# Kernel optimization log

Measured on AMD Instinct MI355X. Metric: run time of the kernel, lower is better.

Reference implementation:

```python
import jax, jax.numpy as jnp
import numpy as np
from jax import lax

RADIUS = 2

def make_kernels(radius):
    # Faithfully reproduces the torch __init__, INCLUDING the bug where
    # NE is computed from the already-normalized NW and SE from SW.
    r = radius
    k = 2 * r + 1
    w = np.ones((k, k), dtype=np.float32)
    L = w.copy(); L[:, r + 1:] = 0
    R = w.copy(); R[:, :r] = 0
    U = w.copy(); U[r + 1:, :] = 0
    D = w.copy(); D[:r, :] = 0
    NW, NE, SW, SE = U.copy(), U.copy(), D.copy(), D.copy()
    half = (r + 1) * k
    L = L / half; R = R / half; U = U / half; D = D / half
    NW[:, r + 1:] = 0
    NE[:, :r] = 0
    SW[:, r + 1:] = 0
    SE[:, :r] = 0
    NW = NW / (r + 1) ** 2
    NE = NW / (r + 1) ** 2  # bug in original: uses new NW
    SW = SW / (r + 1) ** 2
    SE = SW / (r + 1) ** 2  # bug in original: uses new SW
    # order matches d channels 0..7 in forward: L,R,U,D,NW,NE,SW,SE
    return jnp.asarray(np.stack([L, R, U, D, NW, NE, SW, SE])[:, None])  # [8,1,k,k]

def setup_inputs() -> dict:
    key = jax.random.key(0)
    x = jax.random.uniform(key, (8, 3, 768, 768), dtype=jnp.float32)
    return {"x": x, "kernels": make_kernels(RADIUS), "iteration": 3}

def reference(x, kernels, iteration):
    B, C, H, W = x.shape
    k = kernels.shape[-1]
    r = (k - 1) // 2
    # fuse the per-channel loop: treat each (image, channel) as its own sample
    xc = x.reshape(B * C, 1, H, W)

    def step(xc, _):
        # all 8 directional box filters in one conv: [BC,8,H,W]
        conv = lax.conv_general_dilated(
            xc, kernels, window_strides=(1, 1), padding=[(r, r), (r, r)],
            dimension_numbers=("NCHW", "OIHW", "NCHW"))
        d = conv - xc                                   # [BC,8,H,W]
        idx = jnp.argmin(jnp.abs(d), axis=1, keepdims=True)
        dm = jnp.take_along_axis(d, idx, axis=1)        # [BC,1,H,W]
        return xc + dm, None

    xc, _ = lax.scan(step, xc, None, length=iteration)
    return xc.reshape(B, C, H, W)
```

## Files before the change

kernel.cpp:

```cpp
#include <hip/hip_runtime.h>
#include <math.h>


typedef float f4 __attribute__((ext_vector_type(4)));

#define TW 64
#define TH 24

template<int H2, int W2, bool LAST>
__device__ __forceinline__ void step(const float* __restrict__ X,
                                     float* __restrict__ Y,
                                     float* __restrict__ outp,
                                     int gy0, int gx0, int tid) {
    constexpr int PW = W2 + 4;
    const float w15 = 1.0f / 15.0f;
    const float w9  = 1.0f / 9.0f;
    const float w81 = (1.0f / 9.0f) / 9.0f;

    constexpr int SC = W2 / 4;
    constexpr int NSEG = H2 * SC;
    for (int s = tid; s < NSEG; s += 256) {
        const int y  = s / SC;
        const int xs = (s - y * SC) * 4;
        float Wv[5][8];
        #pragma unroll
        for (int r = 0; r < 5; r++) {
            const float* p = X + (y + r) * PW + xs;
            *(f4*)&Wv[r][0] = *(const f4*)p;
            *(f4*)&Wv[r][4] = *(const f4*)(p + 4);
        }
        #pragma unroll
        for (int j = 0; j < 4; j++) {
            const float c = Wv[2][j + 2];
            float aL = 0.0f, aR = 0.0f, aU = 0.0f, aD = 0.0f;
            float aNW = 0.0f, aNE = 0.0f, aSW = 0.0f, aSE = 0.0f;
            #pragma unroll
            for (int r = 0; r < 5; r++)
                #pragma unroll
                for (int cc = 0; cc < 3; cc++)
                    aL = fmaf(w15, Wv[r][j + cc], aL);
            #pragma unroll
            for (int r = 0; r < 5; r++)
                #pragma unroll
                for (int cc = 2; cc < 5; cc++)
                    aR = fmaf(w15, Wv[r][j + cc], aR);
            #pragma unroll
            for (int r = 0; r < 3; r++)
                #pragma unroll
                for (int cc = 0; cc < 5; cc++)
                    aU = fmaf(w15, Wv[r][j + cc], aU);
            #pragma unroll
            for (int r = 2; r < 5; r++)
                #pragma unroll
                for (int cc = 0; cc < 5; cc++)
                    aD = fmaf(w15, Wv[r][j + cc], aD);
            #pragma unroll
            for (int r = 0; r < 3; r++)
                #pragma unroll
                for (int cc = 0; cc < 3; cc++) {
                    aNW = fmaf(w9,  Wv[r][j + cc], aNW);
                    aNE = fmaf(w81, Wv[r][j + cc], aNE);
                }
            #pragma unroll
            for (int r = 2; r < 5; r++)
                #pragma unroll
                for (int cc = 0; cc < 3; cc++) {
                    aSW = fmaf(w9,  Wv[r][j + cc], aSW);
                    aSE = fmaf(w81, Wv[r][j + cc], aSE);
                }

            const float d0 = aL - c, d1 = aR - c, d2 = aU - c, d3 = aD - c;
            const float d4 = aNW - c, d5 = aNE - c, d6 = aSW - c, d7 = aSE - c;

            float best = fabsf(d0), bd = d0, a;
            a = fabsf(d1); if (a < best) { best = a; bd = d1; }
            a = fabsf(d2); if (a < best) { best = a; bd = d2; }
            a = fabsf(d3); if (a < best) { best = a; bd = d3; }
            a = fabsf(d4); if (a < best) { best = a; bd = d4; }
            a = fabsf(d5); if (a < best) { best = a; bd = d5; }
            a = fabsf(d6); if (a < best) { best = a; bd = d6; }
            a = fabsf(d7); if (a < best) { best = a; bd = d7; }

            const float res = c + bd;
            if (LAST) {
                outp[y * 768 + xs + j] = res;
            } else {
                const bool inside = ((unsigned)(gy0 + y) < 768u) &&
                                    ((unsigned)(gx0 + xs + j) < 768u);
                Y[y * W2 + xs + j] = inside ? res : 0.0f;
            }
        }
    }
    __syncthreads();
}

__global__ __launch_bounds__(256) void swf_fused(const float* __restrict__ in,
                                                 float* __restrict__ out) {
    __shared__ __align__(16) float A[36 * 76];
    __shared__ __align__(16) float B[32 * 72];

    const int tid = threadIdx.x;
    const int tx0 = blockIdx.x * TW;
    const int ty0 = blockIdx.y * TH;
    const long long base = (long long)blockIdx.z * (768 * 768);
    const float* inp = in + base;

    for (int i = tid; i < 36 * 76; i += 256) {
        int ly = i / 76, lx = i - ly * 76;
        int gy = ty0 + ly - 6, gx = tx0 + lx - 6;
        float v = 0.0f;
        if ((unsigned)gy < 768u && (unsigned)gx < 768u)
            v = inp[gy * 768 + gx];
        A[i] = v;
    }
    __syncthreads();

    step<32, 72, false>(A, B, nullptr, ty0 - 4, tx0 - 4, tid);
    step<28, 68, false>(B, A, nullptr, ty0 - 2, tx0 - 2, tid);
    step<24, 64, true >(A, nullptr,
                        out + base + (long long)ty0 * 768 + tx0, ty0, tx0, tid);
}

extern "C" void kernel_launch(void* const* d_in, const int* in_sizes, int n_in,
                              void* d_out, int out_size, void* d_ws, size_t ws_size,
                              hipStream_t stream) {
    const float* x = (const float*)d_in[0];
    float* out = (float*)d_out;

    dim3 grid(768 / TW, 768 / TH, 24);
    dim3 block(256);
    swf_fused<<<grid, block, 0, stream>>>(x, out);
}
```

Baseline: 208.6 us.

## Enlarge fused tile to 64x64, vectorize loads/stores, restructure per-row accumulation

Raises tile height from 24 to 64 so the halo recomputation overhead of the three fused iterations shrinks, growing shared memory to 76x76 and 72x72 buffers. Loads the input tile with 2-wide vector reads, writes results as float4, and skips bounds masking for interior tiles. The filter sums are accumulated row by row into 8x4 accumulators and the argmin becomes a tree reduction. The larger shared footprint (about 43KB) and more registers per thread may reduce occupancy, and the grid has fewer blocks.

```diff
diff --git a/kernel.cpp b/kernel.cpp
--- a/kernel.cpp
+++ b/kernel.cpp
@@ -2,10 +2,11 @@
 #include <math.h>
 
 
-typedef float f4 __attribute__((ext_vector_type(4)));
+typedef float f4v __attribute__((ext_vector_type(4)));
+typedef float f2v __attribute__((ext_vector_type(2), aligned(8)));
 
 #define TW 64
-#define TH 24
+#define TH 64
 
 template<int H2, int W2, bool LAST>
 __device__ __forceinline__ void step(const float* __restrict__ X,
@@ -13,82 +14,103 @@
                                      float* __restrict__ outp,
                                      int gy0, int gx0, int tid) {
     constexpr int PW = W2 + 4;
+    constexpr int SC = W2 / 4;
+    constexpr int NSEG = H2 * SC;
     const float w15 = 1.0f / 15.0f;
     const float w9  = 1.0f / 9.0f;
     const float w81 = (1.0f / 9.0f) / 9.0f;
 
-    constexpr int SC = W2 / 4;
-    constexpr int NSEG = H2 * SC;
+    const bool interior = (gy0 >= 0) && (gx0 >= 0) &&
+                          (gy0 + H2 <= 768) && (gx0 + W2 <= 768);
+
     for (int s = tid; s < NSEG; s += 256) {
         const int y  = s / SC;
         const int xs = (s - y * SC) * 4;
-        float Wv[5][8];
+        const float* rp = X + y * PW + xs;
+
+        float acc[8][4];
+        #pragma unroll
+        for (int d = 0; d < 8; d++)
+            #pragma unroll
+            for (int j = 0; j < 4; j++) acc[d][j] = 0.0f;
+        float ctr[4];
+
         #pragma unroll
         for (int r = 0; r < 5; r++) {
-            const float* p = X + (y + r) * PW + xs;
-            *(f4*)&Wv[r][0] = *(const f4*)p;
-            *(f4*)&Wv[r][4] = *(const f4*)(p + 4);
+            const float* p = rp + r * PW;
+            f4v lo = *(const f4v*)p;
+            f4v hi = *(const f4v*)(p + 4);
+            float w[8] = {lo.x, lo.y, lo.z, lo.w, hi.x, hi.y, hi.z, hi.w};
+
+            #pragma unroll
+            for (int j = 0; j < 4; j++) {
+                acc[0][j] = fmaf(w15, w[j + 0], acc[0][j]);
+                acc[0][j] = fmaf(w15, w[j + 1], acc[0][j]);
+                acc[0][j] = fmaf(w15, w[j + 2], acc[0][j]);
+                acc[1][j] = fmaf(w15, w[j + 2], acc[1][j]);
+                acc[1][j] = fmaf(w15, w[j + 3], acc[1][j]);
+                acc[1][j] = fmaf(w15, w[j + 4], acc[1][j]);
+                if (r < 3) {
+                    acc[2][j] = fmaf(w15, w[j + 0], acc[2][j]);
+                    acc[2][j] = fmaf(w15, w[j + 1], acc[2][j]);
+                    acc[2][j] = fmaf(w15, w[j + 2], acc[2][j]);
+                    acc[2][j] = fmaf(w15, w[j + 3], acc[2][j]);
+                    acc[2][j] = fmaf(w15, w[j + 4], acc[2][j]);
+                    acc[4][j] = fmaf(w9,  w[j + 0], acc[4][j]);
+                    acc[4][j] = fmaf(w9,  w[j + 1], acc[4][j]);
+                    acc[4][j] = fmaf(w9,  w[j + 2], acc[4][j]);
+                    acc[5][j] = fmaf(w81, w[j + 0], acc[5][j]);
+                    acc[5][j] = fmaf(w81, w[j + 1], acc[5][j]);
+                    acc[5][j] = fmaf(w81, w[j + 2], acc[5][j]);
+                }
+                if (r >= 2) {
+                    acc[3][j] = fmaf(w15, w[j + 0], acc[3][j]);
+                    acc[3][j] = fmaf(w15, w[j + 1], acc[3][j]);
+                    acc[3][j] = fmaf(w15, w[j + 2], acc[3][j]);
+                    acc[3][j] = fmaf(w15, w[j + 3], acc[3][j]);
+                    acc[3][j] = fmaf(w15, w[j + 4], acc[3][j]);
+                    acc[6][j] = fmaf(w9,  w[j + 0], acc[6][j]);
+                    acc[6][j] = fmaf(w9,  w[j + 1], acc[6][j]);
+                    acc[6][j] = fmaf(w9,  w[j + 2], acc[6][j]);
+                    acc[7][j] = fmaf(w81, w[j + 0], acc[7][j]);
+                    acc[7][j] = fmaf(w81, w[j + 1], acc[7][j]);
+                    acc[7][j] = fmaf(w81, w[j + 2], acc[7][j]);
+                }
+                if (r == 2) ctr[j] = w[j + 2];
+            }
         }
+
+        f4v R;
         #pragma unroll
         for (int j = 0; j < 4; j++) {
-            const float c = Wv[2][j + 2];
-            float aL = 0.0f, aR = 0.0f, aU = 0.0f, aD = 0.0f;
-            float aNW = 0.0f, aNE = 0.0f, aSW = 0.0f, aSE = 0.0f;
-            #pragma unroll
-            for (int r = 0; r < 5; r++)
-                #pragma unroll
-                for (int cc = 0; cc < 3; cc++)
-                    aL = fmaf(w15, Wv[r][j + cc], aL);
-            #pragma unroll
-            for (int r = 0; r < 5; r++)
-                #pragma unroll
-                for (int cc = 2; cc < 5; cc++)
-                    aR = fmaf(w15, Wv[r][j + cc], aR);
-            #pragma unroll
-            for (int r = 0; r < 3; r++)
-                #pragma unroll
-                for (int cc = 0; cc < 5; cc++)
-                    aU = fmaf(w15, Wv[r][j + cc], aU);
-            #pragma unroll
-            for (int r = 2; r < 5; r++)
-                #pragma unroll
-                for (int cc = 0; cc < 5; cc++)
-                    aD = fmaf(w15, Wv[r][j + cc], aD);
-            #pragma unroll
-            for (int r = 0; r < 3; r++)
-                #pragma unroll
-                for (int cc = 0; cc < 3; cc++) {
-                    aNW = fmaf(w9,  Wv[r][j + cc], aNW);
-                    aNE = fmaf(w81, Wv[r][j + cc], aNE);
-                }
-            #pragma unroll
-            for (int r = 2; r < 5; r++)
-                #pragma unroll
-                for (int cc = 0; cc < 3; cc++) {
-                    aSW = fmaf(w9,  Wv[r][j + cc], aSW);
-                    aSE = fmaf(w81, Wv[r][j + cc], aSE);
-                }
+            const float c = ctr[j];
+            const float e0 = acc[0][j] - c, e1 = acc[1][j] - c;
+            const float e2 = acc[2][j] - c, e3 = acc[3][j] - c;
+            const float e4 = acc[4][j] - c, e5 = acc[5][j] - c;
+            const float e6 = acc[6][j] - c, e7 = acc[7][j] - c;
+            float m01 = (fabsf(e1) < fabsf(e0)) ? e1 : e0;
+            float m23 = (fabsf(e3) < fabsf(e2)) ? e3 : e2;
+            float m45 = (fabsf(e5) < fabsf(e4)) ? e5 : e4;
+            float m67 = (fabsf(e7) < fabsf(e6)) ? e7 : e6;
+            float mA  = (fabsf(m23) < fabsf(m01)) ? m23 : m01;
+            float mB  = (fabsf(m67) < fabsf(m45)) ? m67 : m45;
+            float bd  = (fabsf(mB)  < fabsf(mA))  ? mB  : mA;
+            const float res = c + bd;
+            if (j == 0) R.x = res; else if (j == 1) R.y = res;
+            else if (j == 2) R.z = res; else R.w = res;
+        }
 
-            const float d0 = aL - c, d1 = aR - c, d2 = aU - c, d3 = aD - c;
-            const float d4 = aNW - c, d5 = aNE - c, d6 = aSW - c, d7 = aSE - c;
-
-            float best = fabsf(d0), bd = d0, a;
-            a = fabsf(d1); if (a < best) { best = a; bd = d1; }
-            a = fabsf(d2); if (a < best) { best = a; bd = d2; }
-            a = fabsf(d3); if (a < best) { best = a; bd = d3; }
-            a = fabsf(d4); if (a < best) { best = a; bd = d4; }
-            a = fabsf(d5); if (a < best) { best = a; bd = d5; }
-            a = fabsf(d6); if (a < best) { best = a; bd = d6; }
-            a = fabsf(d7); if (a < best) { best = a; bd = d7; }
-
-            const float res = c + bd;
-            if (LAST) {
-                outp[y * 768 + xs + j] = res;
-            } else {
-                const bool inside = ((unsigned)(gy0 + y) < 768u) &&
-                                    ((unsigned)(gx0 + xs + j) < 768u);
-                Y[y * W2 + xs + j] = inside ? res : 0.0f;
-            }
+        if (LAST) {
+            *(f4v*)(outp + y * 768 + xs) = R;
+        } else if (interior) {
+            *(f4v*)(Y + y * W2 + xs) = R;
+        } else {
+            const bool rowin = ((unsigned)(gy0 + y) < 768u);
+            R.x = (rowin && (unsigned)(gx0 + xs + 0) < 768u) ? R.x : 0.0f;
+            R.y = (rowin && (unsigned)(gx0 + xs + 1) < 768u) ? R.y : 0.0f;
+            R.z = (rowin && (unsigned)(gx0 + xs + 2) < 768u) ? R.z : 0.0f;
+            R.w = (rowin && (unsigned)(gx0 + xs + 3) < 768u) ? R.w : 0.0f;
+            *(f4v*)(Y + y * W2 + xs) = R;
         }
     }
     __syncthreads();
@@ -96,8 +118,8 @@
 
 __global__ __launch_bounds__(256) void swf_fused(const float* __restrict__ in,
                                                  float* __restrict__ out) {
-    __shared__ __align__(16) float A[36 * 76];
-    __shared__ __align__(16) float B[32 * 72];
+    __shared__ __align__(16) float A[76 * 76];
+    __shared__ __align__(16) float B[72 * 72];
 
     const int tid = threadIdx.x;
     const int tx0 = blockIdx.x * TW;
@@ -105,19 +127,28 @@
     const long long base = (long long)blockIdx.z * (768 * 768);
     const float* inp = in + base;
 
-    for (int i = tid; i < 36 * 76; i += 256) {
-        int ly = i / 76, lx = i - ly * 76;
-        int gy = ty0 + ly - 6, gx = tx0 + lx - 6;
-        float v = 0.0f;
-        if ((unsigned)gy < 768u && (unsigned)gx < 768u)
-            v = inp[gy * 768 + gx];
-        A[i] = v;
+    for (int i = tid; i < 76 * 38; i += 256) {
+        const int ly  = i / 38;
+        const int lx2 = i - ly * 38;
+        const int gy  = ty0 + ly - 6;
+        const int gx  = tx0 + lx2 * 2 - 6;
+        f2v v = {0.0f, 0.0f};
+        if ((unsigned)gy < 768u) {
+            const float* g = inp + gy * 768 + gx;
+            if ((unsigned)gx < 767u) {
+                v = *(const f2v*)g;
+            } else {
+                if ((unsigned)gx < 768u)       v.x = g[0];
+                if ((unsigned)(gx + 1) < 768u) v.y = g[1];
+            }
+        }
+        *(f2v*)(A + ly * 76 + lx2 * 2) = v;
     }
     __syncthreads();
 
-    step<32, 72, false>(A, B, nullptr, ty0 - 4, tx0 - 4, tid);
-    step<28, 68, false>(B, A, nullptr, ty0 - 2, tx0 - 2, tid);
-    step<24, 64, true >(A, nullptr,
+    step<72, 72, false>(A, B, nullptr, ty0 - 4, tx0 - 4, tid);
+    step<68, 68, false>(B, A, nullptr, ty0 - 2, tx0 - 2, tid);
+    step<64, 64, true >(A, nullptr,
                         out + base + (long long)ty0 * 768 + tx0, ty0, tx0, tid);
 }
 
```

New measurement: 202.2 us. 3.0% less time.
